# Optimization experiments

Measured on AMD Instinct MI355X. Metric: run time of the kernel, lower is better.

Reference implementation:

```python
import jax, jax.numpy as jnp
import numpy as np

N = 100000   # nodes
E = 800000   # main-graph edges
EH = 400000  # hull-graph edges
H = 128      # hidden_channels
F = 128      # num_filters
OE = 256     # out_emb_channels
L2 = 256     # int(cha_scale*OE*(1-cha_rate)) = int(2*256*0.5)
OC = 1       # out_channels


def _W(k, i, o):
    return jax.random.normal(k, (i, o), jnp.float32) / np.sqrt(i).astype(np.float32)


def setup_inputs() -> dict:
    key = jax.random.key(0)
    ks = jax.random.split(key, 24)
    return {
        "e2": jax.random.normal(ks[0], (E, H), jnp.float32),
        "i": jax.random.randint(ks[1], (E,), 0, N),
        "fea_hull": jax.random.normal(ks[2], (EH, 16), jnp.float32),
        "edge_index_hull": jax.random.randint(ks[3], (2, EH), 0, N),
        # parameters (stored [in, out])
        "w_hull": _W(ks[4], H, F),                      # lin_hull, no bias
        "w_mlp0": _W(ks[5], 16, F), "b_mlp0": jnp.zeros((F,), jnp.float32),
        "w_mlp1": _W(ks[6], F, F), "b_mlp1": jnp.zeros((F,), jnp.float32),
        "w1_hull": _W(ks[7], F, H), "b1_hull": jnp.zeros((H,), jnp.float32),
        "w2_hull": _W(ks[8], H, L2), "b2_hull": jnp.zeros((L2,), jnp.float32),
        "w_cat": _W(ks[9], L2 + H, H), "b_cat": jnp.zeros((H,), jnp.float32),
        "w_up": _W(ks[10], H, OE), "b_up": jnp.zeros((OE,), jnp.float32),
        "w_l0": _W(ks[11], OE, OE), "b_l0": jnp.zeros((OE,), jnp.float32),
        "w_l1": _W(ks[12], OE, OE), "b_l1": jnp.zeros((OE,), jnp.float32),
        "w_out": _W(ks[13], OE, OC),                    # lin, no bias
    }


def reference(e2, i, fea_hull, edge_index_hull,
              w_hull, w_mlp0, b_mlp0, w_mlp1, b_mlp1,
              w1_hull, b1_hull, w2_hull, b2_hull,
              w_cat, b_cat, w_up, b_up,
              w_l0, b_l0, w_l1, b_l1, w_out):
    act = jax.nn.silu
    # v = scatter_sum(e2, i) over nodes -> [N, H]
    v = jax.ops.segment_sum(e2, i, num_segments=N)
    j_, i_ = edge_index_hull[0], edge_index_hull[1]
    v_hull = v @ w_hull                                        # [N, F]
    W_h = act(fea_hull @ w_mlp0 + b_mlp0) @ w_mlp1 + b_mlp1    # [EH, F]
    e_hull = v_hull[j_] * W_h                                  # gather-multiply
    out_hull = jax.ops.segment_sum(e_hull, i_, num_segments=N) # scatter-sum
    out_hull = act(out_hull @ w1_hull + b1_hull)
    out_hull = out_hull @ w2_hull + b2_hull                    # [N, L2]
    v = act(jnp.concatenate([v, out_hull], axis=1) @ w_cat + b_cat)
    v = v @ w_up + b_up
    v = act(v @ w_l0 + b_l0)
    v = act(v @ w_l1 + b_l1)
    return v @ w_out                                           # [N, OC]
```

## Files before the change

### kernel.cpp

```cpp
#include <hip/hip_runtime.h>
#include <hip/hip_bf16.h>

typedef __bf16 v8bf __attribute__((ext_vector_type(8)));
typedef __bf16 v4bf __attribute__((ext_vector_type(4)));
typedef float  v4f  __attribute__((ext_vector_type(4)));

__device__ __forceinline__ v8bf zero8() {
    v8bf r;
#pragma unroll
    for (int i = 0; i < 8; ++i) r[i] = (__bf16)0.f;
    return r;
}
__device__ __forceinline__ v4f zero4() { v4f r; r[0]=r[1]=r[2]=r[3]=0.f; return r; }

__device__ __forceinline__ v8bf load8bf(const __bf16* p) { return *(const v8bf*)p; }

__device__ __forceinline__ v8bf load8f(const float* p) {
    const float4 x = ((const float4*)p)[0];
    const float4 y = ((const float4*)p)[1];
    v8bf r;
    r[0]=(__bf16)x.x; r[1]=(__bf16)x.y; r[2]=(__bf16)x.z; r[3]=(__bf16)x.w;
    r[4]=(__bf16)y.x; r[5]=(__bf16)y.y; r[6]=(__bf16)y.z; r[7]=(__bf16)y.w;
    return r;
}
__device__ __forceinline__ float silu_f(float x) { return x / (1.f + __expf(-x)); }

struct TDesc { const float* s; __bf16* d; int K; int N; };
struct TPack { TDesc t[9]; };

__global__ __launch_bounds__(256) void transpose_all(TPack p) {
    TDesc td = p.t[blockIdx.x];
    int total = td.K * td.N;
    for (int idx = blockIdx.y * 256 + threadIdx.x; idx < total; idx += 16 * 256) {
        int k = idx / td.N, n = idx - k * td.N;
        td.d[n * td.K + k] = (__bf16)td.s[idx];
    }
}

__global__ __launch_bounds__(256) void hist_kernel(const int* __restrict__ idx,
                                                   int* __restrict__ counts, int n) {
    int g = blockIdx.x * 256 + threadIdx.x;
    if (g < n) atomicAdd(&counts[idx[g]], 1);
}

__global__ __launch_bounds__(256) void scan_block_sums(const int* __restrict__ counts,
                                                       int* __restrict__ partials, int n) {
    int t = threadIdx.x, b = blockIdx.x;
    int base = b * 2048 + t * 8;
    int s = 0;
#pragma unroll
    for (int i = 0; i < 8; ++i) {
        int g = base + i;
        s += (g < n) ? counts[g] : 0;
    }
#pragma unroll
    for (int off = 32; off; off >>= 1) s += __shfl_down(s, off);
    __shared__ int wsum[4];
    if ((t & 63) == 0) wsum[t >> 6] = s;
    __syncthreads();
    if (t == 0) partials[b] = wsum[0] + wsum[1] + wsum[2] + wsum[3];
}

__global__ void scan_partials_serial(int* __restrict__ partials, int nb,
                                     int* __restrict__ row_start, int n, int total) {
    if (threadIdx.x == 0) {
        int run = 0;
        for (int i = 0; i < nb; ++i) { int t = partials[i]; partials[i] = run; run += t; }
        row_start[n] = total;
    }
}

__global__ __launch_bounds__(256) void scan_write(const int* __restrict__ counts,
                                                  const int* __restrict__ partials,
                                                  int* __restrict__ row_start,
                                                  int* __restrict__ cursor, int n) {
    int t = threadIdx.x, b = blockIdx.x;
    int base = b * 2048 + t * 8;
    int vals[8];
    int tot = 0;
#pragma unroll
    for (int i = 0; i < 8; ++i) {
        int g = base + i;
        vals[i] = (g < n) ? counts[g] : 0;
        tot += vals[i];
    }
    __shared__ int sh[256];
    sh[t] = tot;
    __syncthreads();
#pragma unroll
    for (int d = 1; d < 256; d <<= 1) {
        int v = (t >= d) ? sh[t - d] : 0;
        __syncthreads();
        sh[t] += v;
        __syncthreads();
    }
    int run = partials[b] + sh[t] - tot;
#pragma unroll
    for (int i = 0; i < 8; ++i) {
        int g = base + i;
        if (g < n) { row_start[g] = run; cursor[g] = run; }
        run += vals[i];
    }
}

__global__ __launch_bounds__(256) void rank_scatter(const int* __restrict__ idx,
                                                    int* __restrict__ cursor,
                                                    int* __restrict__ order, int n) {
    int g = blockIdx.x * 256 + threadIdx.x;
    if (g < n) {
        int d = idx[g];
        int pos = atomicAdd(&cursor[d], 1);
        order[pos] = g;
    }
}

__global__ __launch_bounds__(256) void gather_v(const float* __restrict__ e2,
                                                const int* __restrict__ order,
                                                const int* __restrict__ row_start,
                                                __bf16* __restrict__ v, int N) {
    __shared__ float4 red[2][4][32];
    int t = threadIdx.x;
    int half = t >> 7, tl = t & 127;
    int grp = tl >> 5, lane = tl & 31;
    int node = blockIdx.x * 2 + half;
    int nc = (node < N) ? node : N - 1;
    int r0 = row_start[nc], r1 = row_start[nc + 1];
    float4 acc = make_float4(0.f, 0.f, 0.f, 0.f);
    int r = r0 + grp;
    for (; r + 4 < r1; r += 8) {
        int e0 = order[r], e1 = order[r + 4];
        float4 a = *(const float4*)(e2 + (size_t)e0 * 128 + lane * 4);
        float4 b = *(const float4*)(e2 + (size_t)e1 * 128 + lane * 4);
        acc.x += a.x + b.x; acc.y += a.y + b.y;
        acc.z += a.z + b.z; acc.w += a.w + b.w;
    }
    if (r < r1) {
        int e0 = order[r];
        float4 a = *(const float4*)(e2 + (size_t)e0 * 128 + lane * 4);
        acc.x += a.x; acc.y += a.y; acc.z += a.z; acc.w += a.w;
    }
    red[half][grp][lane] = acc;
    __syncthreads();
    if (grp == 0 && node < N) {
        float4 s0 = red[half][0][lane], s1 = red[half][1][lane];
        float4 s2 = red[half][2][lane], s3 = red[half][3][lane];
        v4bf o;
        o[0] = (__bf16)(s0.x + s1.x + s2.x + s3.x);
        o[1] = (__bf16)(s0.y + s1.y + s2.y + s3.y);
        o[2] = (__bf16)(s0.z + s1.z + s2.z + s3.z);
        o[3] = (__bf16)(s0.w + s1.w + s2.w + s3.w);
        *(v4bf*)(v + (size_t)node * 128 + lane * 4) = o;
    }
}

__global__ __launch_bounds__(256) void gather_oh(const __bf16* __restrict__ msg,
                                                 const int* __restrict__ row_start,
                                                 __bf16* __restrict__ oh, int N) {
    int t = threadIdx.x;
    int node = blockIdx.x * 16 + (t >> 4);
    int seg = t & 15;
    if (node >= N) return;
    int r0 = row_start[node], r1 = row_start[node + 1];
    float acc[8] = {0.f, 0.f, 0.f, 0.f, 0.f, 0.f, 0.f, 0.f};
    int r = r0;
    for (; r + 1 < r1; r += 2) {
        v8bf a = *(const v8bf*)(msg + (size_t)r * 128 + seg * 8);
        v8bf b = *(const v8bf*)(msg + (size_t)(r + 1) * 128 + seg * 8);
#pragma unroll
        for (int i = 0; i < 8; ++i) acc[i] += (float)a[i] + (float)b[i];
    }
    if (r < r1) {
        v8bf a = *(const v8bf*)(msg + (size_t)r * 128 + seg * 8);
#pragma unroll
        for (int i = 0; i < 8; ++i) acc[i] += (float)a[i];
    }
    v8bf o;
#pragma unroll
    for (int i = 0; i < 8; ++i) o[i] = (__bf16)acc[i];
    *(v8bf*)(oh + (size_t)node * 128 + seg * 8) = o;
}

__global__ __launch_bounds__(256) void gemm_vhull(const __bf16* __restrict__ v,
                                                  const __bf16* __restrict__ wT,
                                                  __bf16* __restrict__ out, int M) {
    __shared__ __bf16 bS[128 * 136];
    int t = threadIdx.x, wave = t >> 6, lane = t & 63, q = lane >> 4, l16 = lane & 15;
    int m0 = blockIdx.x * 128;
    {
        int row = t >> 1, half = t & 1;
        const v8bf* g = (const v8bf*)(wT + (size_t)row * 128 + half * 64);
        v8bf* d = (v8bf*)(bS + row * 136 + half * 64);
#pragma unroll
        for (int i = 0; i < 8; ++i) d[i] = g[i];
    }
    __syncthreads();
    int r0 = m0 + wave * 32;
    v4f acc[2][8];
#pragma unroll
    for (int i = 0; i < 2; ++i)
#pragma unroll
        for (int j = 0; j < 8; ++j) acc[i][j] = zero4();
    int ar0 = r0 + l16;      if (ar0 >= M) ar0 = M - 1;
    int ar1 = r0 + 16 + l16; if (ar1 >= M) ar1 = M - 1;
#pragma unroll
    for (int kt = 0; kt < 4; ++kt) {
        v8bf a0 = load8bf(v + (size_t)ar0 * 128 + kt * 32 + q * 8);
        v8bf a1 = load8bf(v + (size_t)ar1 * 128 + kt * 32 + q * 8);
#pragma unroll
        for (int nt = 0; nt < 8; ++nt) {
            v8bf b = *(const v8bf*)(bS + (nt * 16 + l16) * 136 + kt * 32 + q * 8);
            acc[0][nt] = __builtin_amdgcn_mfma_f32_16x16x32_bf16(a0, b, acc[0][nt], 0, 0, 0);
            acc[1][nt] = __builtin_amdgcn_mfma_f32_16x16x32_bf16(a1, b, acc[1][nt], 0, 0, 0);
        }
    }
#pragma unroll
    for (int tile = 0; tile < 2; ++tile)
#pragma unroll
        for (int nt = 0; nt < 8; ++nt)
#pragma unroll
            for (int r = 0; r < 4; ++r) {
                int row = r0 + tile * 16 + q * 4 + r;
                if (row < M) out[(size_t)row * 128 + nt * 16 + l16] = (__bf16)acc[tile][nt][r];
            }
}

__global__ __launch_bounds__(256) void hull_msg(const float* __restrict__ fea,
                                                const int* __restrict__ perm,
                                                const int* __restrict__ jidx,
                                                const __bf16* __restrict__ w0T,
                                                const float* __restrict__ bias0,
                                                const __bf16* __restrict__ w1T,
                                                const float* __restrict__ bias1,
                                                const __bf16* __restrict__ vhull,
                                                __bf16* __restrict__ msg, int EH) {
    __shared__ __bf16 hb[64][136];
    __shared__ __bf16 whS[64][136];
    __shared__ int jb[64];
    int t = threadIdx.x;
    int wave = t >> 6, lane = t & 63, q = lane >> 4, l16 = lane & 15;
    int r0 = blockIdx.x * 64;
    if (t < 64) {
        int slot = r0 + t; if (slot >= EH) slot = EH - 1;
        jb[t] = jidx[perm[slot]];
    }
    {
        int slot = r0 + wave * 16 + l16; if (slot >= EH) slot = EH - 1;
        int e = perm[slot];
        v8bf a = (q < 2) ? load8f(fea + (size_t)e * 16 + q * 8) : zero8();
        v4f acc[8];
#pragma unroll
        for (int i = 0; i < 8; ++i) acc[i] = zero4();
#pragma unroll
        for (int nt = 0; nt < 8; ++nt) {
            v8bf b = (q < 2) ? load8bf(w0T + (size_t)(nt * 16 + l16) * 16 + q * 8) : zero8();
            acc[nt] = __builtin_amdgcn_mfma_f32_16x16x32_bf16(a, b, acc[nt], 0, 0, 0);
        }
#pragma unroll
        for (int nt = 0; nt < 8; ++nt) {
            int col = nt * 16 + l16;
            float bc = bias0[col];
#pragma unroll
            for (int r = 0; r < 4; ++r) {
                int rowL = wave * 16 + q * 4 + r;
                hb[rowL][col] = (__bf16)silu_f(acc[nt][r] + bc);
            }
        }
    }
    __syncthreads();
    {
        v8bf af[4];
#pragma unroll
        for (int kt = 0; kt < 4; ++kt)
            af[kt] = *(const v8bf*)&hb[wave * 16 + l16][kt * 32 + q * 8];
        v4f acc[8];
#pragma unroll
        for (int i = 0; i < 8; ++i) acc[i] = zero4();
#pragma unroll
        for (int kt = 0; kt < 4; ++kt)
#pragma unroll
            for (int nt = 0; nt < 8; ++nt) {
                v8bf b = load8bf(w1T + (size_t)(nt * 16 + l16) * 128 + kt * 32 + q * 8);
                acc[nt] = __builtin_amdgcn_mfma_f32_16x16x32_bf16(af[kt], b, acc[nt], 0, 0, 0);
            }
#pragma unroll
        for (int nt = 0; nt < 8; ++nt) {
            int col = nt * 16 + l16;
            float bc = bias1[col];
#pragma unroll
            for (int r = 0; r < 4; ++r) {
                int rowL = wave * 16 + q * 4 + r;
                whS[rowL][col] = (__bf16)(acc[nt][r] + bc);
            }
        }
    }
    __syncthreads();
    {
        int row = t >> 2, sub = t & 3;
        int slot = r0 + row;
        if (slot < EH) {
            int j = jb[row];
            const v8bf* vr = (const v8bf*)(vhull + (size_t)j * 128 + sub * 32);
            v8bf* mp = (v8bf*)(msg + (size_t)slot * 128 + sub * 32);
#pragma unroll
            for (int i = 0; i < 4; ++i) {
                v8bf wv = *(const v8bf*)&whS[row][sub * 32 + i * 8];
                v8bf vv = vr[i];
                v8bf o;
#pragma unroll
                for (int k = 0; k < 8; ++k) o[k] = (__bf16)((float)wv[k] * (float)vv[k]);
                mp[i] = o;
            }
        }
    }
}

#define ALD 392
#define BLD 392

template<int K, int NCH, bool SILU>
__device__ __forceinline__ void gemm_stage(const __bf16* __restrict__ wT,
                                           const float* __restrict__ bias,
                                           __bf16* actS, __bf16* bS,
                                           int srcCol, int dstCol,
                                           int wave, int lane, int t) {
    int q = lane >> 4, l16 = lane & 15;
    v4f acc[NCH * 4];
#pragma unroll
    for (int j = 0; j < NCH * 4; ++j) acc[j] = zero4();

    int brow = t >> 3, sub = t & 7;
#pragma unroll
    for (int c = 0; c < NCH; ++c) {
        {
            const v8bf* g = (const v8bf*)(wT + (size_t)(c * 64 + brow) * K) + sub * (K / 64);
            v8bf* d = (v8bf*)(bS + brow * BLD) + sub * (K / 64);
#pragma unroll
            for (int i = 0; i < K / 64; ++i) d[i] = g[i];
        }
        __syncthreads();
#pragma unroll
        for (int kt = 0; kt < K / 32; ++kt) {
            v8bf a0 = *(const v8bf*)(actS + (wave * 16 + l16) * ALD + srcCol + kt * 32 + q * 8);
#pragma unroll
            for (int nt = 0; nt < 4; ++nt) {
                v8bf b = *(const v8bf*)(bS + (nt * 16 + l16) * BLD + kt * 32 + q * 8);
                acc[c * 4 + nt] = __builtin_amdgcn_mfma_f32_16x16x32_bf16(a0, b, acc[c * 4 + nt], 0, 0, 0);
            }
        }
        __syncthreads();
    }
#pragma unroll
    for (int j = 0; j < NCH * 4; ++j) {
        float bc = bias[j * 16 + l16];
#pragma unroll
        for (int r = 0; r < 4; ++r) {
            int row = wave * 16 + q * 4 + r;
            float val = acc[j][r] + bc;
            if (SILU) val = silu_f(val);
            actS[row * ALD + dstCol + j * 16 + l16] = (__bf16)val;
        }
    }
}

__global__ __launch_bounds__(512, 1) void node_chain(
    const __bf16* __restrict__ v, const __bf16* __restrict__ oh,
    const __bf16* __restrict__ w1T, const float* __restrict__ b1,
    const __bf16* __restrict__ w2T, const float* __restrict__ b2,
    const __bf16* __restrict__ wcatT, const float* __restrict__ bcat,
    const __bf16* __restrict__ wupT, const float* __restrict__ bup,
    const __bf16* __restrict__ wl0T, const float* __restrict__ bl0,
    const __bf16* __restrict__ wl1T, const float* __restrict__ bl1,
    const float* __restrict__ wout, float* __restrict__ out, int M) {
    __shared__ __bf16 actS[128 * ALD];
    __shared__ __bf16 bS[64 * BLD];
    int t = threadIdx.x, wave = t >> 6, lane = t & 63;
    int m0b = blockIdx.x * 128;

    {
        int row = wave * 16 + (lane >> 2), quarter = lane & 3;
        int gr = m0b + row; if (gr >= M) gr = M - 1;
        const v8bf* sv = (const v8bf*)(v + (size_t)gr * 128 + quarter * 32);
        const v8bf* so = (const v8bf*)(oh + (size_t)gr * 128 + quarter * 32);
        v8bf* dv = (v8bf*)(actS + row * ALD + quarter * 32);
        v8bf* doh = (v8bf*)(actS + row * ALD + 256 + quarter * 32);
#pragma unroll
        for (int i = 0; i < 4; ++i) { dv[i] = sv[i]; doh[i] = so[i]; }
    }

    gemm_stage<128, 2, true >(w1T,   b1,   actS, bS, 256, 128, wave, lane, t);
    gemm_stage<128, 4, false>(w2T,   b2,   actS, bS, 128, 128, wave, lane, t);
    gemm_stage<384, 2, true >(wcatT, bcat, actS, bS, 0,   0,   wave, lane, t);
    gemm_stage<128, 4, false>(wupT,  bup,  actS, bS, 0,   128, wave, lane, t);
    gemm_stage<256, 4, true >(wl0T,  bl0,  actS, bS, 128, 128, wave, lane, t);
    gemm_stage<256, 4, true >(wl1T,  bl1,  actS, bS, 128, 128, wave, lane, t);

    {
        int row = wave * 16 + (lane >> 2), quarter = lane & 3;
        const __bf16* ap = actS + row * ALD + 128 + quarter * 64;
        const float* wq = wout + quarter * 64;
        float s = 0.f;
#pragma unroll
        for (int c8 = 0; c8 < 8; ++c8) {
            v8bf a8 = *(const v8bf*)(ap + c8 * 8);
            const float4 w0 = ((const float4*)(wq + c8 * 8))[0];
            const float4 w1 = ((const float4*)(wq + c8 * 8))[1];
            s += (float)a8[0] * w0.x + (float)a8[1] * w0.y + (float)a8[2] * w0.z + (float)a8[3] * w0.w;
            s += (float)a8[4] * w1.x + (float)a8[5] * w1.y + (float)a8[6] * w1.z + (float)a8[7] * w1.w;
        }
        s += __shfl_xor(s, 1);
        s += __shfl_xor(s, 2);
        int gr = m0b + row;
        if (quarter == 0 && gr < M) out[gr] = s;
    }
}

static inline char* align16(char* p) {
    return (char*)(((uintptr_t)p + 15) & ~(uintptr_t)15);
}

extern "C" void kernel_launch(void* const* d_in, const int* in_sizes, int n_in,
                              void* d_out, int out_size, void* d_ws, size_t ws_size,
                              hipStream_t stream) {
    const float* e2      = (const float*)d_in[0];
    const int*   iidx    = (const int*)d_in[1];
    const float* fea     = (const float*)d_in[2];
    const int*   eih     = (const int*)d_in[3];
    const float* w_hull  = (const float*)d_in[4];
    const float* w_mlp0  = (const float*)d_in[5];
    const float* b_mlp0  = (const float*)d_in[6];
    const float* w_mlp1  = (const float*)d_in[7];
    const float* b_mlp1  = (const float*)d_in[8];
    const float* w1_hull = (const float*)d_in[9];
    const float* b1_hull = (const float*)d_in[10];
    const float* w2_hull = (const float*)d_in[11];
    const float* b2_hull = (const float*)d_in[12];
    const float* w_cat   = (const float*)d_in[13];
    const float* b_cat   = (const float*)d_in[14];
    const float* w_up    = (const float*)d_in[15];
    const float* b_up    = (const float*)d_in[16];
    const float* w_l0    = (const float*)d_in[17];
    const float* b_l0    = (const float*)d_in[18];
    const float* w_l1    = (const float*)d_in[19];
    const float* b_l1    = (const float*)d_in[20];
    const float* w_out   = (const float*)d_in[21];

    int N  = out_size;
    int E  = in_sizes[0] / 128;
    int EH = in_sizes[2] / 16;
    const int* jidx_h = eih;
    const int* iidx_h = eih + EH;

    char* p = (char*)d_ws;
    __bf16* v     = (__bf16*)p; p += (size_t)N * 128 * 2;
    __bf16* oh    = (__bf16*)p; p += (size_t)N * 128 * 2;
    __bf16* vhull = (__bf16*)p; p += (size_t)N * 128 * 2;
    __bf16* wp = (__bf16*)p;
    __bf16* w_hullT = wp; wp += 128 * 128;
    __bf16* w0T     = wp; wp += 128 * 16;
    __bf16* w1mT    = wp; wp += 128 * 128;
    __bf16* w1hT    = wp; wp += 128 * 128;
    __bf16* w2hT    = wp; wp += 256 * 128;
    __bf16* wcatT   = wp; wp += 128 * 384;
    __bf16* wupT    = wp; wp += 256 * 128;
    __bf16* wl0T    = wp; wp += 256 * 256;
    __bf16* wl1T    = wp; wp += 256 * 256;
    p = align16((char*)wp);
    int* counts   = (int*)p; p += (size_t)N * 4;
    int* counts2  = (int*)p; p += (size_t)N * 4;
    int* row_s    = (int*)p; p += (size_t)(N + 1) * 4;
    int* cursor   = (int*)p; p += (size_t)N * 4;
    int* row2     = (int*)p; p += (size_t)(N + 1) * 4;
    int* cursor2  = (int*)p; p += (size_t)N * 4;
    int* order    = (int*)p; p += (size_t)E * 4;
    int* perm2    = (int*)p; p += (size_t)EH * 4;
    int* partials = (int*)p; p += 256 * 4;
    p = align16(p);
    size_t need_msg = (size_t)EH * 128 * 2;
    __bf16* msg;
    if ((size_t)(p - (char*)d_ws) + need_msg <= ws_size) msg = (__bf16*)p;
    else                                                 msg = (__bf16*)d_in[0];

    TPack tp;
    tp.t[0] = { w_hull,  w_hullT, 128, 128 };
    tp.t[1] = { w_mlp0,  w0T,      16, 128 };
    tp.t[2] = { w_mlp1,  w1mT,    128, 128 };
    tp.t[3] = { w1_hull, w1hT,    128, 128 };
    tp.t[4] = { w2_hull, w2hT,    128, 256 };
    tp.t[5] = { w_cat,   wcatT,   384, 128 };
    tp.t[6] = { w_up,    wupT,    128, 256 };
    tp.t[7] = { w_l0,    wl0T,    256, 256 };
    tp.t[8] = { w_l1,    wl1T,    256, 256 };
    transpose_all<<<dim3(9, 16), 256, 0, stream>>>(tp);

    (void)hipMemsetAsync(counts, 0, (size_t)N * 4 * 2, stream);

    const int nbS = (N + 2047) / 2048;

    hist_kernel<<<(E + 255) / 256, 256, 0, stream>>>(iidx, counts, E);
    scan_block_sums<<<nbS, 256, 0, stream>>>(counts, partials, N);
    scan_partials_serial<<<1, 64, 0, stream>>>(partials, nbS, row_s, N, E);
    scan_write<<<nbS, 256, 0, stream>>>(counts, partials, row_s, cursor, N);
    rank_scatter<<<(E + 255) / 256, 256, 0, stream>>>(iidx, cursor, order, E);

    gather_v<<<(N + 1) / 2, 256, 0, stream>>>(e2, order, row_s, v, N);

    gemm_vhull<<<(N + 127) / 128, 256, 0, stream>>>(v, w_hullT, vhull, N);

    hist_kernel<<<(EH + 255) / 256, 256, 0, stream>>>(iidx_h, counts2, EH);
    scan_block_sums<<<nbS, 256, 0, stream>>>(counts2, partials, N);
    scan_partials_serial<<<1, 64, 0, stream>>>(partials, nbS, row2, N, EH);
    scan_write<<<nbS, 256, 0, stream>>>(counts2, partials, row2, cursor2, N);
    rank_scatter<<<(EH + 255) / 256, 256, 0, stream>>>(iidx_h, cursor2, perm2, EH);

    hull_msg<<<(EH + 63) / 64, 256, 0, stream>>>(fea, perm2, jidx_h, w0T, b_mlp0,
                                                 w1mT, b_mlp1, vhull, msg, EH);
    gather_oh<<<(N + 15) / 16, 256, 0, stream>>>(msg, row2, oh, N);

    node_chain<<<(N + 127) / 128, 512, 0, stream>>>(v, oh, w1hT, b1_hull, w2hT, b2_hull,
                                                    wcatT, b_cat, wupT, b_up,
                                                    wl0T, b_l0, wl1T, b_l1,
                                                    w_out, (float*)d_out, N);
}
```

Before: 1.136 ms.

## Fuse hull scatter into message kernel, batch CSR builds, prefetch GEMM weights

Builds both CSR structures (main and hull) in shared batched kernels instead of two separate sequences, and replaces the serial partial scan with a wave-level shuffle scan. The hull message kernel now reduces its sorted rows in shared memory by destination and atomically adds segment sums into an fp32 node buffer. This removes the bf16 message buffer round trip and the separate gather kernel. The node_chain GEMM stage also prefetches the next weight chunk into registers while computing. It adds a 51MB memset and fp32 atomics in exchange.

```diff
diff --git a/kernel.cpp b/kernel.cpp
--- a/kernel.cpp
+++ b/kernel.cpp
@@ -37,21 +37,28 @@
     }
 }
 
-__global__ __launch_bounds__(256) void hist_kernel(const int* __restrict__ idx,
-                                                   int* __restrict__ counts, int n) {
+__global__ __launch_bounds__(256) void hist_both(const int* __restrict__ idxE,
+                                                 const int* __restrict__ idxH,
+                                                 int* __restrict__ countsE,
+                                                 int* __restrict__ countsH,
+                                                 int E, int EH) {
     int g = blockIdx.x * 256 + threadIdx.x;
-    if (g < n) atomicAdd(&counts[idx[g]], 1);
+    if (g < E) atomicAdd(&countsE[idxE[g]], 1);
+    else if (g < E + EH) atomicAdd(&countsH[idxH[g - E]], 1);
 }
 
 __global__ __launch_bounds__(256) void scan_block_sums(const int* __restrict__ counts,
-                                                       int* __restrict__ partials, int n) {
+                                                       int* __restrict__ partials,
+                                                       int n, int nbS) {
     int t = threadIdx.x, b = blockIdx.x;
-    int base = b * 2048 + t * 8;
+    const int* src = counts + ((b >= nbS) ? n : 0);
+    int bb = (b >= nbS) ? b - nbS : b;
+    int base = bb * 2048 + t * 8;
     int s = 0;
 #pragma unroll
     for (int i = 0; i < 8; ++i) {
         int g = base + i;
-        s += (g < n) ? counts[g] : 0;
+        s += (g < n) ? src[g] : 0;
     }
 #pragma unroll
     for (int off = 32; off; off >>= 1) s += __shfl_down(s, off);
@@ -61,27 +68,48 @@
     if (t == 0) partials[b] = wsum[0] + wsum[1] + wsum[2] + wsum[3];
 }
 
-__global__ void scan_partials_serial(int* __restrict__ partials, int nb,
-                                     int* __restrict__ row_start, int n, int total) {
-    if (threadIdx.x == 0) {
+__global__ void scan_partials_two(int* __restrict__ partials, int nb,
+                                  int* __restrict__ row_s, int* __restrict__ row2,
+                                  int N, int E, int EH) {
+    int w = threadIdx.x >> 6, lane = threadIdx.x & 63;
+    if (w > 1) return;
+    int* p = partials + w * nb;
+    if (nb <= 64) {
+        int v = (lane < nb) ? p[lane] : 0;
+        int orig = v;
+#pragma unroll
+        for (int d = 1; d < 64; d <<= 1) {
+            int u = __shfl_up(v, d);
+            if (lane >= d) v += u;
+        }
+        if (lane < nb) p[lane] = v - orig;
+    } else if (lane == 0) {
         int run = 0;
-        for (int i = 0; i < nb; ++i) { int t = partials[i]; partials[i] = run; run += t; }
-        row_start[n] = total;
-    }
+        for (int i = 0; i < nb; ++i) { int tv = p[i]; p[i] = run; run += tv; }
+    }
+    if (lane == 0) { if (w == 0) row_s[N] = E; else row2[N] = EH; }
 }
 
 __global__ __launch_bounds__(256) void scan_write(const int* __restrict__ counts,
                                                   const int* __restrict__ partials,
-                                                  int* __restrict__ row_start,
-                                                  int* __restrict__ cursor, int n) {
+                                                  int* __restrict__ row_s,
+                                                  int* __restrict__ cursor,
+                                                  int* __restrict__ row2,
+                                                  int* __restrict__ cursor2,
+                                                  int n, int nbS) {
     int t = threadIdx.x, b = blockIdx.x;
-    int base = b * 2048 + t * 8;
+    bool hull = b >= nbS;
+    const int* src = counts + (hull ? n : 0);
+    int bb = hull ? b - nbS : b;
+    int* rs = hull ? row2 : row_s;
+    int* cu = hull ? cursor2 : cursor;
+    int base = bb * 2048 + t * 8;
     int vals[8];
     int tot = 0;
 #pragma unroll
     for (int i = 0; i < 8; ++i) {
         int g = base + i;
-        vals[i] = (g < n) ? counts[g] : 0;
+        vals[i] = (g < n) ? src[g] : 0;
         tot += vals[i];
     }
     __shared__ int sh[256];
@@ -98,19 +126,30 @@
 #pragma unroll
     for (int i = 0; i < 8; ++i) {
         int g = base + i;
-        if (g < n) { row_start[g] = run; cursor[g] = run; }
+        if (g < n) { rs[g] = run; cu[g] = run; }
         run += vals[i];
     }
 }
 
-__global__ __launch_bounds__(256) void rank_scatter(const int* __restrict__ idx,
-                                                    int* __restrict__ cursor,
-                                                    int* __restrict__ order, int n) {
+__global__ __launch_bounds__(256) void rank_scatter_both(const int* __restrict__ idxE,
+                                                         const int* __restrict__ idxH,
+                                                         int* __restrict__ cursorE,
+                                                         int* __restrict__ cursorH,
+                                                         int* __restrict__ order,
+                                                         int* __restrict__ perm2,
+                                                         int* __restrict__ dests2,
+                                                         int E, int EH) {
     int g = blockIdx.x * 256 + threadIdx.x;
-    if (g < n) {
-        int d = idx[g];
-        int pos = atomicAdd(&cursor[d], 1);
+    if (g < E) {
+        int d = idxE[g];
+        int pos = atomicAdd(&cursorE[d], 1);
         order[pos] = g;
+    } else if (g < E + EH) {
+        int e = g - E;
+        int d = idxH[e];
+        int pos = atomicAdd(&cursorH[d], 1);
+        perm2[pos] = e;
+        dests2[pos] = d;
     }
 }
 
@@ -153,33 +192,6 @@
     }
 }
 
-__global__ __launch_bounds__(256) void gather_oh(const __bf16* __restrict__ msg,
-                                                 const int* __restrict__ row_start,
-                                                 __bf16* __restrict__ oh, int N) {
-    int t = threadIdx.x;
-    int node = blockIdx.x * 16 + (t >> 4);
-    int seg = t & 15;
-    if (node >= N) return;
-    int r0 = row_start[node], r1 = row_start[node + 1];
-    float acc[8] = {0.f, 0.f, 0.f, 0.f, 0.f, 0.f, 0.f, 0.f};
-    int r = r0;
-    for (; r + 1 < r1; r += 2) {
-        v8bf a = *(const v8bf*)(msg + (size_t)r * 128 + seg * 8);
-        v8bf b = *(const v8bf*)(msg + (size_t)(r + 1) * 128 + seg * 8);
-#pragma unroll
-        for (int i = 0; i < 8; ++i) acc[i] += (float)a[i] + (float)b[i];
-    }
-    if (r < r1) {
-        v8bf a = *(const v8bf*)(msg + (size_t)r * 128 + seg * 8);
-#pragma unroll
-        for (int i = 0; i < 8; ++i) acc[i] += (float)a[i];
-    }
-    v8bf o;
-#pragma unroll
-    for (int i = 0; i < 8; ++i) o[i] = (__bf16)acc[i];
-    *(v8bf*)(oh + (size_t)node * 128 + seg * 8) = o;
-}
-
 __global__ __launch_bounds__(256) void gemm_vhull(const __bf16* __restrict__ v,
                                                   const __bf16* __restrict__ wT,
                                                   __bf16* __restrict__ out, int M) {
@@ -227,21 +239,25 @@
 __global__ __launch_bounds__(256) void hull_msg(const float* __restrict__ fea,
                                                 const int* __restrict__ perm,
                                                 const int* __restrict__ jidx,
+                                                const int* __restrict__ dests,
                                                 const __bf16* __restrict__ w0T,
                                                 const float* __restrict__ bias0,
                                                 const __bf16* __restrict__ w1T,
                                                 const float* __restrict__ bias1,
                                                 const __bf16* __restrict__ vhull,
-                                                __bf16* __restrict__ msg, int EH) {
+                                                float* __restrict__ oh32, int EH) {
     __shared__ __bf16 hb[64][136];
     __shared__ __bf16 whS[64][136];
     __shared__ int jb[64];
+    __shared__ int db[64];
     int t = threadIdx.x;
     int wave = t >> 6, lane = t & 63, q = lane >> 4, l16 = lane & 15;
     int r0 = blockIdx.x * 64;
     if (t < 64) {
-        int slot = r0 + t; if (slot >= EH) slot = EH - 1;
-        jb[t] = jidx[perm[slot]];
+        int slot = r0 + t;
+        int sc = (slot < EH) ? slot : EH - 1;
+        jb[t] = jidx[perm[sc]];
+        db[t] = (slot < EH) ? dests[slot] : -1;
     }
     {
         int slot = r0 + wave * 16 + l16; if (slot >= EH) slot = EH - 1;
@@ -300,7 +316,6 @@
         if (slot < EH) {
             int j = jb[row];
             const v8bf* vr = (const v8bf*)(vhull + (size_t)j * 128 + sub * 32);
-            v8bf* mp = (v8bf*)(msg + (size_t)slot * 128 + sub * 32);
 #pragma unroll
             for (int i = 0; i < 4; ++i) {
                 v8bf wv = *(const v8bf*)&whS[row][sub * 32 + i * 8];
@@ -308,9 +323,24 @@
                 v8bf o;
 #pragma unroll
                 for (int k = 0; k < 8; ++k) o[k] = (__bf16)((float)wv[k] * (float)vv[k]);
-                mp[i] = o;
-            }
-        }
+                *(v8bf*)&whS[row][sub * 32 + i * 8] = o;
+            }
+        }
+    }
+    __syncthreads();
+    {
+        int c = t & 127, half = t >> 7;
+        int rbeg = half * 32, rend = rbeg + 32;
+        float run = 0.f; int cur = -1;
+        for (int r = rbeg; r < rend; ++r) {
+            int d = db[r];
+            if (d != cur) {
+                if (cur >= 0) atomicAdd(oh32 + (size_t)cur * 128 + c, run);
+                run = 0.f; cur = d;
+            }
+            if (cur >= 0) run += (float)whS[r][c];
+        }
+        if (cur >= 0) atomicAdd(oh32 + (size_t)cur * 128 + c, run);
     }
 }
 
@@ -329,15 +359,29 @@
     for (int j = 0; j < NCH * 4; ++j) acc[j] = zero4();
 
     int brow = t >> 3, sub = t & 7;
+    constexpr int RV = K / 64;
+    v8bf breg[RV];
+    {
+        const v8bf* g = (const v8bf*)(wT + (size_t)brow * K) + sub * RV;
+#pragma unroll
+        for (int i = 0; i < RV; ++i) breg[i] = g[i];
+    }
 #pragma unroll
     for (int c = 0; c < NCH; ++c) {
+        __syncthreads();
         {
-            const v8bf* g = (const v8bf*)(wT + (size_t)(c * 64 + brow) * K) + sub * (K / 64);
-            v8bf* d = (v8bf*)(bS + brow * BLD) + sub * (K / 64);
-#pragma unroll
-            for (int i = 0; i < K / 64; ++i) d[i] = g[i];
-        }
-        __syncthreads();
+            v8bf* d = (v8bf*)(bS + brow * BLD) + sub * RV;
+#pragma unroll
+            for (int i = 0; i < RV; ++i) d[i] = breg[i];
+        }
+        if (c + 1 < NCH) {
+            const v8bf* g = (const v8bf*)(wT + (size_t)((c + 1) * 64 + brow) * K) + sub * RV;
+#pragma unroll
+            for (int i = 0; i < RV; ++i) breg[i] = g[i];
+        }
+        asm volatile("s_waitcnt lgkmcnt(0)" ::: "memory");
+        __builtin_amdgcn_s_barrier();
+        __builtin_amdgcn_sched_barrier(0);
 #pragma unroll
         for (int kt = 0; kt < K / 32; ++kt) {
             v8bf a0 = *(const v8bf*)(actS + (wave * 16 + l16) * ALD + srcCol + kt * 32 + q * 8);
@@ -347,7 +391,6 @@
                 acc[c * 4 + nt] = __builtin_amdgcn_mfma_f32_16x16x32_bf16(a0, b, acc[c * 4 + nt], 0, 0, 0);
             }
         }
-        __syncthreads();
     }
 #pragma unroll
     for (int j = 0; j < NCH * 4; ++j) {
@@ -363,7 +406,7 @@
 }
 
 __global__ __launch_bounds__(512, 1) void node_chain(
-    const __bf16* __restrict__ v, const __bf16* __restrict__ oh,
+    const __bf16* __restrict__ v, const float* __restrict__ oh,
     const __bf16* __restrict__ w1T, const float* __restrict__ b1,
     const __bf16* __restrict__ w2T, const float* __restrict__ b2,
     const __bf16* __restrict__ wcatT, const float* __restrict__ bcat,
@@ -380,11 +423,11 @@
         int row = wave * 16 + (lane >> 2), quarter = lane & 3;
         int gr = m0b + row; if (gr >= M) gr = M - 1;
         const v8bf* sv = (const v8bf*)(v + (size_t)gr * 128 + quarter * 32);
-        const v8bf* so = (const v8bf*)(oh + (size_t)gr * 128 + quarter * 32);
+        const float* so = oh + (size_t)gr * 128 + quarter * 32;
         v8bf* dv = (v8bf*)(actS + row * ALD + quarter * 32);
         v8bf* doh = (v8bf*)(actS + row * ALD + 256 + quarter * 32);
 #pragma unroll
-        for (int i = 0; i < 4; ++i) { dv[i] = sv[i]; doh[i] = so[i]; }
+        for (int i = 0; i < 4; ++i) { dv[i] = sv[i]; doh[i] = load8f(so + i * 8); }
     }
 
     gemm_stage<128, 2, true >(w1T,   b1,   actS, bS, 256, 128, wave, lane, t);
@@ -452,8 +495,8 @@
 
     char* p = (char*)d_ws;
     __bf16* v     = (__bf16*)p; p += (size_t)N * 128 * 2;
-    __bf16* oh    = (__bf16*)p; p += (size_t)N * 128 * 2;
     __bf16* vhull = (__bf16*)p; p += (size_t)N * 128 * 2;
+    float*  oh32  = (float*)p;  p += (size_t)N * 128 * 4;
     __bf16* wp = (__bf16*)p;
     __bf16* w_hullT = wp; wp += 128 * 128;
     __bf16* w0T     = wp; wp += 128 * 16;
@@ -465,20 +508,16 @@
     __bf16* wl0T    = wp; wp += 256 * 256;
     __bf16* wl1T    = wp; wp += 256 * 256;
     p = align16((char*)wp);
-    int* counts   = (int*)p; p += (size_t)N * 4;
-    int* counts2  = (int*)p; p += (size_t)N * 4;
+    int* counts   = (int*)p; p += (size_t)N * 4 * 2;
     int* row_s    = (int*)p; p += (size_t)(N + 1) * 4;
     int* cursor   = (int*)p; p += (size_t)N * 4;
     int* row2     = (int*)p; p += (size_t)(N + 1) * 4;
     int* cursor2  = (int*)p; p += (size_t)N * 4;
     int* order    = (int*)p; p += (size_t)E * 4;
     int* perm2    = (int*)p; p += (size_t)EH * 4;
-    int* partials = (int*)p; p += 256 * 4;
-    p = align16(p);
-    size_t need_msg = (size_t)EH * 128 * 2;
-    __bf16* msg;
-    if ((size_t)(p - (char*)d_ws) + need_msg <= ws_size) msg = (__bf16*)p;
-    else                                                 msg = (__bf16*)d_in[0];
+    int* dests2   = (int*)p; p += (size_t)EH * 4;
+    int* partials = (int*)p; p += 512 * 4;
+    int* counts2  = counts + N;
 
     TPack tp;
     tp.t[0] = { w_hull,  w_hullT, 128, 128 };
@@ -493,30 +532,25 @@
     transpose_all<<<dim3(9, 16), 256, 0, stream>>>(tp);
 
     (void)hipMemsetAsync(counts, 0, (size_t)N * 4 * 2, stream);
+    (void)hipMemsetAsync(oh32, 0, (size_t)N * 128 * 4, stream);
 
     const int nbS = (N + 2047) / 2048;
 
-    hist_kernel<<<(E + 255) / 256, 256, 0, stream>>>(iidx, counts, E);
-    scan_block_sums<<<nbS, 256, 0, stream>>>(counts, partials, N);
-    scan_partials_serial<<<1, 64, 0, stream>>>(partials, nbS, row_s, N, E);
-    scan_write<<<nbS, 256, 0, stream>>>(counts, partials, row_s, cursor, N);
-    rank_scatter<<<(E + 255) / 256, 256, 0, stream>>>(iidx, cursor, order, E);
+    hist_both<<<(E + EH + 255) / 256, 256, 0, stream>>>(iidx, iidx_h, counts, counts2, E, EH);
+    scan_block_sums<<<2 * nbS, 256, 0, stream>>>(counts, partials, N, nbS);
+    scan_partials_two<<<1, 128, 0, stream>>>(partials, nbS, row_s, row2, N, E, EH);
+    scan_write<<<2 * nbS, 256, 0, stream>>>(counts, partials, row_s, cursor, row2, cursor2, N, nbS);
+    rank_scatter_both<<<(E + EH + 255) / 256, 256, 0, stream>>>(iidx, iidx_h, cursor, cursor2,
+                                                                order, perm2, dests2, E, EH);
 
     gather_v<<<(N + 1) / 2, 256, 0, stream>>>(e2, order, row_s, v, N);
 
     gemm_vhull<<<(N + 127) / 128, 256, 0, stream>>>(v, w_hullT, vhull, N);
 
-    hist_kernel<<<(EH + 255) / 256, 256, 0, stream>>>(iidx_h, counts2, EH);
-    scan_block_sums<<<nbS, 256, 0, stream>>>(counts2, partials, N);
-    scan_partials_serial<<<1, 64, 0, stream>>>(partials, nbS, row2, N, EH);
-    scan_write<<<nbS, 256, 0, stream>>>(counts2, partials, row2, cursor2, N);
-    rank_scatter<<<(EH + 255) / 256, 256, 0, stream>>>(iidx_h, cursor2, perm2, EH);
-
-    hull_msg<<<(EH + 63) / 64, 256, 0, stream>>>(fea, perm2, jidx_h, w0T, b_mlp0,
-                                                 w1mT, b_mlp1, vhull, msg, EH);
-    gather_oh<<<(N + 15) / 16, 256, 0, stream>>>(msg, row2, oh, N);
-
-    node_chain<<<(N + 127) / 128, 512, 0, stream>>>(v, oh, w1hT, b1_hull, w2hT, b2_hull,
+    hull_msg<<<(EH + 63) / 64, 256, 0, stream>>>(fea, perm2, jidx_h, dests2, w0T, b_mlp0,
+                                                 w1mT, b_mlp1, vhull, oh32, EH);
+
+    node_chain<<<(N + 127) / 128, 512, 0, stream>>>(v, oh32, w1hT, b1_hull, w2hT, b2_hull,
                                                     wcatT, b_cat, wupT, b_up,
                                                     wl0T, b_l0, wl1T, b_l1,
                                                     w_out, (float*)d_out, N);
```

New measurement: 1.117 ms. About the same (-1.7%).
